# Kernel optimization log

Hardware: AMD Instinct MI355X
Metric: run time of the kernel (lower is better)

## Reference

```python
import jax, jax.numpy as jnp
import numpy as np

EPS = 1e-5
THRESHOLD = 0.7   # ternary threshold factor
QMAX = 127.0      # 2**(act_bits-1) - 1 for act_bits=8


def setup_inputs() -> dict:
    key = jax.random.key(0)
    k1, k2 = jax.random.split(key)
    B, S, D_IN, D_OUT = 4, 8192, 1024, 1024
    x = jax.random.normal(k1, (B, S, D_IN), dtype=jnp.float32)
    weight = jax.random.normal(k2, (D_OUT, D_IN), dtype=jnp.float32) * np.sqrt(2.0 / D_IN)
    gamma = jnp.ones((D_IN,), dtype=jnp.float32)
    beta = jnp.zeros((D_IN,), dtype=jnp.float32)
    return {"x": x, "weight": weight, "gamma": gamma, "beta": beta}


def _fake_quant_act(x):
    # symmetric per-tensor int8 absmax fake quantization (dequantized)
    scale = jnp.maximum(jnp.max(jnp.abs(x)), 1e-8) / QMAX
    q = jnp.round(jnp.clip(x / scale, -QMAX, QMAX)) * scale
    return x + jax.lax.stop_gradient(q - x)  # STE


def _ternary_quant_weight(w):
    # BitNet W1.58: delta = threshold * mean|W|; alpha = mean|W| over kept entries
    absw = jnp.abs(w)
    delta = THRESHOLD * jnp.mean(absw)
    mask = (absw > delta).astype(w.dtype)
    alpha = jnp.sum(absw * mask) / jnp.maximum(jnp.sum(mask), 1.0)
    wq = alpha * jnp.sign(w) * mask
    return w + jax.lax.stop_gradient(wq - w)  # STE


def reference(x, weight, gamma, beta):
    # LayerNorm over last dim
    mu = jnp.mean(x, axis=-1, keepdims=True)
    var = jnp.mean(jnp.square(x - mu), axis=-1, keepdims=True)
    xn = (x - mu) * jax.lax.rsqrt(var + EPS) * gamma + beta
    xq = _fake_quant_act(xn)          # [B, S, D_in]
    wq = _ternary_quant_weight(weight)  # [D_out, D_in]
    return jnp.einsum('bsi,oi->bso', xq, wq)
```

## Files before the change

kernel.cpp:

```cpp
#include <hip/hip_runtime.h>
#include <hip/hip_bf16.h>


#define M_ROWS   32768
#define D_IN     1024
#define D_OUT    1024
#define W_ELEMS  (1024*1024)

typedef __attribute__((ext_vector_type(4))) int int4v;


__global__ __launch_bounds__(256) void ln_stats_wsum_kernel(
    const float* __restrict__ x, const float* __restrict__ gamma,
    const float* __restrict__ beta, float* __restrict__ mu_out,
    float* __restrict__ rstd_out, float* __restrict__ amax_part,
    const float* __restrict__ w, double* __restrict__ wsum_part) {
  __shared__ float wm[4];
  __shared__ double ls[4];
  int t = threadIdx.x;
  int wave = t >> 6, lane = t & 63;

  if (blockIdx.x >= 256) {
    int bln = blockIdx.x - 256;
    int wgid = bln * 4 + wave;
    float4 g[4], b[4];
    #pragma unroll
    for (int k = 0; k < 4; k++) {
      g[k] = ((const float4*)gamma)[lane + 64 * k];
      b[k] = ((const float4*)beta )[lane + 64 * k];
    }
    float amax = 0.0f;
    #pragma unroll 2
    for (int i = 0; i < 8; i++) {
      int row = wgid + 4096 * i;
      const float4* xr = (const float4*)(x + (size_t)row * D_IN);
      float4 v[4];
      #pragma unroll
      for (int k = 0; k < 4; k++) v[k] = xr[lane + 64 * k];
      float s = 0.0f, sq = 0.0f;
      #pragma unroll
      for (int k = 0; k < 4; k++) {
        s  += v[k].x + v[k].y + v[k].z + v[k].w;
        sq += v[k].x*v[k].x + v[k].y*v[k].y + v[k].z*v[k].z + v[k].w*v[k].w;
      }
      #pragma unroll
      for (int off = 1; off < 64; off <<= 1) {
        s  += __shfl_xor(s,  off, 64);
        sq += __shfl_xor(sq, off, 64);
      }
      float mu   = s * (1.0f / D_IN);
      float var  = sq * (1.0f / D_IN) - mu * mu;
      float rstd = rsqrtf(var + 1e-5f);
      if (lane == 0) { mu_out[row] = mu; rstd_out[row] = rstd; }
      #pragma unroll
      for (int k = 0; k < 4; k++) {
        float nx = (v[k].x - mu) * rstd * g[k].x + b[k].x;
        float ny = (v[k].y - mu) * rstd * g[k].y + b[k].y;
        float nz = (v[k].z - mu) * rstd * g[k].z + b[k].z;
        float nw = (v[k].w - mu) * rstd * g[k].w + b[k].w;
        amax = fmaxf(amax, fmaxf(fmaxf(fabsf(nx), fabsf(ny)),
                                 fmaxf(fabsf(nz), fabsf(nw))));
      }
    }
    #pragma unroll
    for (int off = 1; off < 64; off <<= 1)
      amax = fmaxf(amax, __shfl_xor(amax, off, 64));
    if (lane == 0) wm[wave] = amax;
    __syncthreads();
    if (t == 0)
      amax_part[bln] = fmaxf(fmaxf(wm[0], wm[1]), fmaxf(wm[2], wm[3]));
  } else {
    int base = blockIdx.x * 1024 + t;
    double s = 0.0;
    #pragma unroll
    for (int j = 0; j < 4; j++) {
      float4 v = ((const float4*)w)[base + 256 * j];
      s += (double)fabsf(v.x) + (double)fabsf(v.y) +
           (double)fabsf(v.z) + (double)fabsf(v.w);
    }
    #pragma unroll
    for (int off = 1; off < 64; off <<= 1) s += __shfl_xor(s, off, 64);
    if (lane == 0) ls[wave] = s;
    __syncthreads();
    if (t == 0) wsum_part[blockIdx.x] = ((ls[0] + ls[1]) + ls[2]) + ls[3];
  }
}

__global__ __launch_bounds__(256) void wquant_actquant_kernel(
    const float* __restrict__ w, const double* __restrict__ wsum_part,
    signed char* __restrict__ qw, double* __restrict__ ks_part,
    int* __restrict__ kc_part,
    const float* __restrict__ x, const float* __restrict__ gamma,
    const float* __restrict__ beta, const float* __restrict__ mu_arr,
    const float* __restrict__ rstd_arr,
    const float* __restrict__ amax_part, signed char* __restrict__ qx) {
  int t = threadIdx.x;
  int wave = t >> 6, lane = t & 63;

  if (blockIdx.x < 256) {
    __shared__ double lsum[4];
    __shared__ double lss[4];
    __shared__ int    lcc[4];
    double sp = wsum_part[t];
    #pragma unroll
    for (int off = 1; off < 64; off <<= 1) sp += __shfl_xor(sp, off, 64);
    if (lane == 0) lsum[wave] = sp;
    __syncthreads();
    double sumw = ((lsum[0] + lsum[1]) + lsum[2]) + lsum[3];
    double delta = 0.7 * sumw * (1.0 / (double)W_ELEMS);

    int base = blockIdx.x * 1024 + t;
    double ks = 0.0;
    int kc = 0;
    #pragma unroll
    for (int j = 0; j < 4; j++) {
      float4 v = ((const float4*)w)[base + 256 * j];
      char4 q;
      {
        double a = (double)fabsf(v.x); bool m = a > delta;
        q.x = m ? (v.x > 0.0f ? 1 : -1) : 0; if (m) { ks += a; kc++; }
      }
      {
        double a = (double)fabsf(v.y); bool m = a > delta;
        q.y = m ? (v.y > 0.0f ? 1 : -1) : 0; if (m) { ks += a; kc++; }
      }
      {
        double a = (double)fabsf(v.z); bool m = a > delta;
        q.z = m ? (v.z > 0.0f ? 1 : -1) : 0; if (m) { ks += a; kc++; }
      }
      {
        double a = (double)fabsf(v.w); bool m = a > delta;
        q.w = m ? (v.w > 0.0f ? 1 : -1) : 0; if (m) { ks += a; kc++; }
      }
      ((char4*)qw)[base + 256 * j] = q;
    }
    #pragma unroll
    for (int off = 1; off < 64; off <<= 1) {
      ks += __shfl_xor(ks, off, 64);
      kc += __shfl_xor(kc, off, 64);
    }
    if (lane == 0) { lss[wave] = ks; lcc[wave] = kc; }
    __syncthreads();
    if (t == 0) {
      ks_part[blockIdx.x] = ((lss[0] + lss[1]) + lss[2]) + lss[3];
      kc_part[blockIdx.x] = ((lcc[0] + lcc[1]) + lcc[2]) + lcc[3];
    }
  } else {
    __shared__ float lam[4];
    float am = fmaxf(fmaxf(amax_part[t], amax_part[t + 256]),
                     fmaxf(amax_part[t + 512], amax_part[t + 768]));
    #pragma unroll
    for (int off = 1; off < 64; off <<= 1)
      am = fmaxf(am, __shfl_xor(am, off, 64));
    if (lane == 0) lam[wave] = am;
    __syncthreads();
    am = fmaxf(fmaxf(lam[0], lam[1]), fmaxf(lam[2], lam[3]));
    float scale = fmaxf(am, 1e-8f) / 127.0f;

    float4 g = ((const float4*)gamma)[t];
    float4 b = ((const float4*)beta)[t];
    int bid2 = blockIdx.x - 256;
    #pragma unroll 2
    for (int i = 0; i < 16; i++) {
      int row = bid2 * 16 + i;
      float mu = mu_arr[row], rstd = rstd_arr[row];
      float4 v = ((const float4*)(x + (size_t)row * D_IN))[t];
      float nx = ((v.x - mu) * rstd * g.x + b.x) / scale;
      float ny = ((v.y - mu) * rstd * g.y + b.y) / scale;
      float nz = ((v.z - mu) * rstd * g.z + b.z) / scale;
      float nw = ((v.w - mu) * rstd * g.w + b.w) / scale;
      char4 q;
      q.x = (signed char)(int)rintf(fminf(fmaxf(nx, -127.0f), 127.0f));
      q.y = (signed char)(int)rintf(fminf(fmaxf(ny, -127.0f), 127.0f));
      q.z = (signed char)(int)rintf(fminf(fmaxf(nz, -127.0f), 127.0f));
      q.w = (signed char)(int)rintf(fminf(fmaxf(nw, -127.0f), 127.0f));
      ((char4*)(qx + (size_t)row * D_IN))[t] = q;
    }
  }
}


__device__ __forceinline__ void stage16(const signed char* src, signed char* dst) {
  __builtin_amdgcn_global_load_lds(
      (const __attribute__((address_space(1))) unsigned int*)src,
      (__attribute__((address_space(3))) unsigned int*)dst, 16, 0, 0);
}

#define BAR()   __builtin_amdgcn_s_barrier()
#define BARS()  { __builtin_amdgcn_s_barrier(); __builtin_amdgcn_sched_barrier(0); }
#define LGKM0() { asm volatile("s_waitcnt lgkmcnt(0)" ::: "memory"); __builtin_amdgcn_sched_barrier(0); }
#define VMW(N)  { asm volatile("s_waitcnt vmcnt(" #N ")" ::: "memory"); __builtin_amdgcn_sched_barrier(0); }

#define STAGE_A(BUF, HALF, KB) { \
  signed char* d_ = ldsA + (((BUF)*2 + (HALF)) << 14) + (tid << 4); \
  const signed char* s_ = Asrc + (size_t)(HALF) * (128 * D_IN) + (KB); \
  stage16(s_, d_); stage16(s_ + 64 * D_IN, d_ + 8192); }

#define STAGE_B(BUF, HALF, KB) { \
  signed char* d_ = ldsB + (((BUF)*2 + (HALF)) << 14) + (tid << 4); \
  const signed char* s_ = Bsrc + (size_t)(HALF) * (128 * D_IN) + (KB); \
  stage16(s_, d_); stage16(s_ + 64 * D_IN, d_ + 8192); }

#define LOAD_A(P, RH) { _Pragma("unroll") \
  for (int f_ = 0; f_ < 4; f_++) { \
    const signed char* rp_ = (P) + (((RH)*64 + f_*16 + lrow) << 7); \
    a[f_][0] = *(const int4v*)(rp_ + kA0); \
    a[f_][1] = *(const int4v*)(rp_ + kA1); } }

#define LOAD_B(P, CH) { _Pragma("unroll") \
  for (int g_ = 0; g_ < 2; g_++) { \
    const signed char* rp_ = (P) + ((bro + (CH)*32 + g_*16 + lrow) << 7); \
    b[CH][g_][0] = *(const int4v*)(rp_ + kA0); \
    b[CH][g_][1] = *(const int4v*)(rp_ + kA1); } }

#define MFMA_Q(RH, CH) { _Pragma("unroll") \
  for (int f_ = 0; f_ < 4; f_++) { _Pragma("unroll") \
    for (int g_ = 0; g_ < 2; g_++) { \
      acc[(RH)*4+f_][(CH)*2+g_] = __builtin_amdgcn_mfma_i32_16x16x64_i8( \
          a[f_][0], b[CH][g_][0], acc[(RH)*4+f_][(CH)*2+g_], 0, 0, 0); \
      acc[(RH)*4+f_][(CH)*2+g_] = __builtin_amdgcn_mfma_i32_16x16x64_i8( \
          a[f_][1], b[CH][g_][1], acc[(RH)*4+f_][(CH)*2+g_], 0, 0, 0); } } }

#define KITER(FULL, koO, koE2, koO2) \
   \
  LOAD_A(pA0, 0); LOAD_B(pB0, 0); \
  STAGE_B(1, 1, koO); STAGE_A(1, 1, koO); \
  asm volatile("s_waitcnt lgkmcnt(8)" ::: "memory"); \
  BAR(); LGKM0(); \
  __builtin_amdgcn_s_setprio(1); MFMA_Q(0, 0); __builtin_amdgcn_s_setprio(0); BARS(); \
   \
  LOAD_B(pB0, 1); BAR(); LGKM0(); \
  __builtin_amdgcn_s_setprio(1); MFMA_Q(0, 1); __builtin_amdgcn_s_setprio(0); BARS(); \
   \
  LOAD_A(pA0, 1); if (FULL) { STAGE_B(0, 0, koE2); } BAR(); LGKM0(); \
  __builtin_amdgcn_s_setprio(1); MFMA_Q(1, 0); __builtin_amdgcn_s_setprio(0); BARS(); \
   \
  if (FULL) { STAGE_B(0, 1, koE2); STAGE_A(0, 0, koE2); } BAR(); \
  __builtin_amdgcn_s_setprio(1); MFMA_Q(1, 1); __builtin_amdgcn_s_setprio(0); \
  if (FULL) { VMW(6); } else { VMW(0); } BARS(); \
   \
  LOAD_A(pA1, 0); LOAD_B(pB1, 0); if (FULL) { STAGE_A(0, 1, koE2); } \
  asm volatile("s_waitcnt lgkmcnt(8)" ::: "memory"); \
  BAR(); LGKM0(); \
  __builtin_amdgcn_s_setprio(1); MFMA_Q(0, 0); __builtin_amdgcn_s_setprio(0); BARS(); \
   \
  LOAD_B(pB1, 1); BAR(); LGKM0(); \
  __builtin_amdgcn_s_setprio(1); MFMA_Q(0, 1); __builtin_amdgcn_s_setprio(0); BARS(); \
   \
  LOAD_A(pA1, 1); if (FULL) { STAGE_B(1, 0, koO2); } BAR(); LGKM0(); \
  __builtin_amdgcn_s_setprio(1); MFMA_Q(1, 0); __builtin_amdgcn_s_setprio(0); BARS(); \
   \
  if (FULL) { STAGE_A(1, 0, koO2); } BAR(); \
  __builtin_amdgcn_s_setprio(1); MFMA_Q(1, 1); __builtin_amdgcn_s_setprio(0); \
  if (FULL) { VMW(4); } BARS();

__global__ __launch_bounds__(512, 2) void gemm_i8_256_kernel(
    const signed char* __restrict__ A,
    const signed char* __restrict__ B,
    float* __restrict__ C,
    const float* __restrict__ amax_part,
    const double* __restrict__ ks_part, const int* __restrict__ kc_part) {
  extern __shared__ __align__(16) signed char lds[];
  signed char* ldsA = lds;
  signed char* ldsB = lds + 65536;

  const int tid = threadIdx.x;
  const int lane = tid & 63;
  const int wid = tid >> 6;
  const int wr = wid >> 2;
  const int wc = wid & 3;

  int wg = ((blockIdx.x & 7) << 6) + (blockIdx.x >> 3);
  const int m0 = (wg >> 2) << 8;
  const int n0 = (wg & 3) << 8;

  float fscale;
  {
    double* lred = (double*)lds;
    float*  lam  = (float*)(lds + 64);
    int*    lkc  = (int*)(lds + 96);
    float amv = fmaxf(amax_part[tid], amax_part[tid + 512]);
    double ksv = (tid < 256) ? ks_part[tid] : 0.0;
    int    kcv = (tid < 256) ? kc_part[tid] : 0;
    #pragma unroll
    for (int off = 1; off < 64; off <<= 1) {
      amv = fmaxf(amv, __shfl_xor(amv, off, 64));
      ksv += __shfl_xor(ksv, off, 64);
      kcv += __shfl_xor(kcv, off, 64);
    }
    if (lane == 0) { lred[wid] = ksv; lam[wid] = amv; lkc[wid] = kcv; }
    __syncthreads();
    double ksum = 0.0; int kcnt = 0; float am = 0.0f;
    for (int wv = 0; wv < 8; wv++) {
      ksum += lred[wv]; kcnt += lkc[wv]; am = fmaxf(am, lam[wv]);
    }
    double alpha = ksum / (double)((kcnt > 1) ? kcnt : 1);
    fscale = (float)(((double)fmaxf(am, 1e-8f) / 127.0) * alpha);
    __syncthreads();
  }
  asm volatile("s_waitcnt vmcnt(0) lgkmcnt(0)" ::: "memory");
  __builtin_amdgcn_sched_barrier(0);

  int so = (tid << 4) ^ (((tid >> 5) & 1) << 5);
  int r0 = so >> 7, c0 = so & 127;
  const signed char* Asrc = A + (size_t)(m0 + r0) * D_IN + c0;
  const signed char* Bsrc = B + (size_t)(n0 + r0) * D_IN + c0;

  const int lrow = lane & 15;
  const int kA0 = ((lane >> 4) << 4) ^ (((lrow >> 2) & 1) << 5);
  const int kA1 = 64 + kA0;
  const int bro = (wc & 1) << 6;
  const signed char* pA0 = ldsA + (wr << 14);
  const signed char* pA1 = pA0 + 32768;
  const signed char* pB0 = ldsB + ((wc >> 1) << 14);
  const signed char* pB1 = pB0 + 32768;

  int4v acc[8][4] = {};
  int4v a[4][2];
  int4v b[2][2][2];

  STAGE_B(0, 0, 0); STAGE_B(0, 1, 0);
  STAGE_A(0, 0, 0); STAGE_A(0, 1, 0);
  STAGE_B(1, 0, 128); STAGE_A(1, 0, 128);
  VMW(4); BARS();

  for (int i = 0; i < 3; i++) {
    int koO  = (2 * i + 1) * 128;
    int koE2 = (2 * i + 2) * 128;
    int koO2 = (2 * i + 3) * 128;
    KITER(1, koO, koE2, koO2)
  }
  {
    int koO = 7 * 128;
    KITER(0, koO, 0, 0)
  }

  const int crow0 = m0 + (wr << 7) + ((lane >> 4) << 2);
  const int ccol0 = n0 + (wc << 6) + (lane & 15);
  #pragma unroll
  for (int rf = 0; rf < 8; rf++)
    #pragma unroll
    for (int cf = 0; cf < 4; cf++)
      #pragma unroll
      for (int rr = 0; rr < 4; rr++) {
        int row = crow0 + rf * 16 + rr;
        C[(size_t)row * D_OUT + ccol0 + cf * 16] = (float)acc[rf][cf][rr] * fscale;
      }
}

extern "C" void kernel_launch(void* const* d_in, const int* in_sizes, int n_in,
                              void* d_out, int out_size, void* d_ws, size_t ws_size,
                              hipStream_t stream) {
  const float* x     = (const float*)d_in[0];
  const float* w     = (const float*)d_in[1];
  const float* gamma = (const float*)d_in[2];
  const float* beta  = (const float*)d_in[3];
  float* out = (float*)d_out;

  char* ws = (char*)d_ws;
  double* wsum_part = (double*)(ws + 256);
  float*  amax_part = (float*)(ws + 4096);
  double* ks_part   = (double*)(ws + 8192);
  int*    kc_part   = (int*)(ws + 10240);
  float* mu   = (float*)(ws + 16384);
  float* rstd = (float*)(ws + 147456);
  signed char* qw = (signed char*)(ws + 278528);
  signed char* qx = (signed char*)(ws + 1327104);

  ln_stats_wsum_kernel<<<1280, 256, 0, stream>>>(x, gamma, beta, mu, rstd,
                                                 amax_part, w, wsum_part);
  wquant_actquant_kernel<<<2304, 256, 0, stream>>>(w, wsum_part, qw, ks_part,
                                                   kc_part, x, gamma, beta, mu,
                                                   rstd, amax_part, qx);
  gemm_i8_256_kernel<<<512, 512, 131072, stream>>>(qx, qw, out, amax_part,
                                                   ks_part, kc_part);
}
```

Before: 294.0 us.

## Switch int8 GEMM to 32x32x32 MFMA tiles with new LDS swizzle

Replaces the 16x16x64 int8 MFMA inner tiles with 32x32x32 int8 MFMA, reorganising register fragments, the LDS XOR swizzle used for staging and reading, and the epilogue index mapping. Larger MFMA tiles cut the number of LDS fragment reads and MFMA issues per output element, which should improve operand reuse. The risk is higher register pressure from 16-wide accumulators and possible new LDS bank conflicts from the changed swizzle.

After: 295.1 us. No clear change (+0.4%).

```diff
diff --git a/kernel.cpp b/kernel.cpp
--- a/kernel.cpp
+++ b/kernel.cpp
@@ -7,7 +7,8 @@
 #define D_OUT    1024
 #define W_ELEMS  (1024*1024)
 
-typedef __attribute__((ext_vector_type(4))) int int4v;
+typedef __attribute__((ext_vector_type(4)))  int int4v;
+typedef __attribute__((ext_vector_type(16))) int int16v;
 
 
 __global__ __launch_bounds__(256) void ln_stats_wsum_kernel(
@@ -202,24 +203,21 @@
   stage16(s_, d_); stage16(s_ + 64 * D_IN, d_ + 8192); }
 
 #define LOAD_A(P, RH) { _Pragma("unroll") \
-  for (int f_ = 0; f_ < 4; f_++) { \
-    const signed char* rp_ = (P) + (((RH)*64 + f_*16 + lrow) << 7); \
-    a[f_][0] = *(const int4v*)(rp_ + kA0); \
-    a[f_][1] = *(const int4v*)(rp_ + kA1); } }
+  for (int f_ = 0; f_ < 2; f_++) { _Pragma("unroll") \
+    for (int kk_ = 0; kk_ < 4; kk_++) { \
+      a32[f_][kk_] = *(const int4v*)((P) + (((RH)*64 + f_*32 + lrow32) << 7) \
+                     + ((((kk_ << 1) | khalf) ^ rxor) << 4)); } } }
 
 #define LOAD_B(P, CH) { _Pragma("unroll") \
-  for (int g_ = 0; g_ < 2; g_++) { \
-    const signed char* rp_ = (P) + ((bro + (CH)*32 + g_*16 + lrow) << 7); \
-    b[CH][g_][0] = *(const int4v*)(rp_ + kA0); \
-    b[CH][g_][1] = *(const int4v*)(rp_ + kA1); } }
+  for (int kk_ = 0; kk_ < 4; kk_++) { \
+    b32[CH][kk_] = *(const int4v*)((P) + ((bro + (CH)*32 + lrow32) << 7) \
+                   + ((((kk_ << 1) | khalf) ^ rxor) << 4)); } }
 
 #define MFMA_Q(RH, CH) { _Pragma("unroll") \
-  for (int f_ = 0; f_ < 4; f_++) { _Pragma("unroll") \
-    for (int g_ = 0; g_ < 2; g_++) { \
-      acc[(RH)*4+f_][(CH)*2+g_] = __builtin_amdgcn_mfma_i32_16x16x64_i8( \
-          a[f_][0], b[CH][g_][0], acc[(RH)*4+f_][(CH)*2+g_], 0, 0, 0); \
-      acc[(RH)*4+f_][(CH)*2+g_] = __builtin_amdgcn_mfma_i32_16x16x64_i8( \
-          a[f_][1], b[CH][g_][1], acc[(RH)*4+f_][(CH)*2+g_], 0, 0, 0); } } }
+  for (int f_ = 0; f_ < 2; f_++) { _Pragma("unroll") \
+    for (int kk_ = 0; kk_ < 4; kk_++) { \
+      acc32[(RH)*2+f_][CH] = __builtin_amdgcn_mfma_i32_32x32x32_i8( \
+          a32[f_][kk_], b32[CH][kk_], acc32[(RH)*2+f_][CH], 0, 0, 0); } } }
 
 #define KITER(FULL, koO, koE2, koO2) \
    \
@@ -301,23 +299,23 @@
   asm volatile("s_waitcnt vmcnt(0) lgkmcnt(0)" ::: "memory");
   __builtin_amdgcn_sched_barrier(0);
 
-  int so = (tid << 4) ^ (((tid >> 5) & 1) << 5);
+  int so = (tid << 4) ^ (((tid >> 3) & 7) << 4);
   int r0 = so >> 7, c0 = so & 127;
   const signed char* Asrc = A + (size_t)(m0 + r0) * D_IN + c0;
   const signed char* Bsrc = B + (size_t)(n0 + r0) * D_IN + c0;
 
-  const int lrow = lane & 15;
-  const int kA0 = ((lane >> 4) << 4) ^ (((lrow >> 2) & 1) << 5);
-  const int kA1 = 64 + kA0;
+  const int lrow32 = lane & 31;
+  const int khalf  = lane >> 5;
+  const int rxor   = lrow32 & 7;
   const int bro = (wc & 1) << 6;
   const signed char* pA0 = ldsA + (wr << 14);
   const signed char* pA1 = pA0 + 32768;
   const signed char* pB0 = ldsB + ((wc >> 1) << 14);
   const signed char* pB1 = pB0 + 32768;
 
-  int4v acc[8][4] = {};
-  int4v a[4][2];
-  int4v b[2][2][2];
+  int16v acc32[4][2] = {};
+  int4v a32[2][4];
+  int4v b32[2][4];
 
   STAGE_B(0, 0, 0); STAGE_B(0, 1, 0);
   STAGE_A(0, 0, 0); STAGE_A(0, 1, 0);
@@ -335,17 +333,19 @@
     KITER(0, koO, 0, 0)
   }
 
-  const int crow0 = m0 + (wr << 7) + ((lane >> 4) << 2);
-  const int ccol0 = n0 + (wc << 6) + (lane & 15);
   #pragma unroll
-  for (int rf = 0; rf < 8; rf++)
-    #pragma unroll
-    for (int cf = 0; cf < 4; cf++)
-      #pragma unroll
-      for (int rr = 0; rr < 4; rr++) {
-        int row = crow0 + rf * 16 + rr;
-        C[(size_t)row * D_OUT + ccol0 + cf * 16] = (float)acc[rf][cf][rr] * fscale;
-      }
+  for (int rf = 0; rf < 4; rf++) {
+    const int TR = m0 + (wr << 7) + rf * 32 + 4 * khalf;
+    #pragma unroll
+    for (int cf = 0; cf < 2; cf++) {
+      const int TC = n0 + (wc << 6) + cf * 32 + lrow32;
+      #pragma unroll
+      for (int reg = 0; reg < 16; reg++) {
+        int row = TR + (reg & 3) + 8 * (reg >> 2);
+        C[(size_t)row * D_OUT + TC] = (float)acc32[rf][cf][reg] * fscale;
+      }
+    }
+  }
 }
 
 extern "C" void kernel_launch(void* const* d_in, const int* in_sizes, int n_in,
```
